# Optimization experiments

Hardware: AMD Instinct MI355X
Metric: run time of the kernel (lower is better)

Reference implementation:

```python
import jax
import jax.numpy as jnp
import numpy as np

N_NODES = 4096
N_EDGES = 65536
D_FEAT = 64


def setup_inputs() -> dict:
    key = jax.random.key(0)
    k1, k2, k3, k4 = jax.random.split(key, 4)
    x = jax.random.normal(k1, (N_NODES, D_FEAT), dtype=jnp.float32)
    edge_index = jax.random.randint(k2, (2, N_EDGES), 0, N_NODES, dtype=jnp.int32)
    batch = jnp.zeros((N_NODES,), dtype=jnp.int32)
    # GraphConv(in_channels, 1): lin_rel (with bias) on aggregated neighbors, lin_root on self
    w_rel = jax.random.normal(k3, (D_FEAT, 1), dtype=jnp.float32) * 0.1
    w_root = jax.random.normal(k4, (D_FEAT, 1), dtype=jnp.float32) * 0.1
    b = jnp.zeros((1,), dtype=jnp.float32)
    return {"x": x, "edge_index": edge_index, "batch": batch,
            "w_rel": w_rel, "w_root": w_root, "b": b}


def _merge_stars(x, src0, dst0, score):
    """Faithful sequential greedy star contraction (priority order by score desc)."""
    N = x.shape[0]
    order = jnp.argsort(-score)  # descending, ties like argsort

    def step(carry, node):
        xc, src, dst, remaining, center = carry
        active = remaining[node]
        # dests = set of targets of edges whose (current, rewritten) source == node,
        # minus already-chosen center nodes
        dest_edge = src == node                                  # [E]
        dest_node = jnp.zeros(N, bool).at[dst].max(dest_edge)    # node-level set
        dest_node = dest_node & ~center
        # torch does sum over list(dests)+[node]: node counted again (even on self-loop)
        combine = jnp.einsum('n,nd->d', dest_node.astype(xc.dtype), xc) + xc[node]
        D = dest_node.at[node].set(True)                         # dests U {node}
        x2 = xc.at[node].set(combine)
        src2 = jnp.where(D[src], node, src)                      # np.isin rewrite
        dst2 = jnp.where(D[dst], node, dst)
        rem2 = remaining & ~dest_node
        cen2 = center.at[node].set(True)
        carry2 = (jnp.where(active, x2, xc),
                  jnp.where(active, src2, src),
                  jnp.where(active, dst2, dst),
                  jnp.where(active, rem2, remaining),
                  jnp.where(active, cen2, center))
        return carry2, None

    init = (x, src0, dst0, jnp.ones(N, bool), jnp.zeros(N, bool))
    (x_final, _, _, remaining, _), _ = jax.lax.scan(step, init, order)
    return x_final, remaining


def reference(x, edge_index, batch, w_rel, w_root, b):
    N, d = x.shape
    src0, dst0 = edge_index[0], edge_index[1]
    # GraphConv score: W_rel * sum_{j->i} x_j + b + W_root * x_i ; dropout p=0; tanh
    agg = jax.ops.segment_sum(x[src0], dst0, num_segments=N)     # [N, d]
    score = jnp.tanh((agg @ w_rel + x @ w_root + b).reshape(-1)) # [N]

    x_final, remaining = _merge_stars(x, src0, dst0, score)

    # perm = sorted(nodes_remaining); outputs padded to static size N (sentinel -1)
    perm = jnp.nonzero(remaining, size=N, fill_value=N)[0]
    x_pooled = jnp.take(x_final, perm, axis=0, mode='fill', fill_value=0.0)
    kept = perm < N
    batch_pooled = jnp.where(kept, jnp.take(batch, jnp.minimum(perm, N - 1)), -1)
    # filter_adj on the ORIGINAL edge_index: keep edges with both endpoints kept,
    # relabel nodes to their rank among kept nodes; invalid edges -> -1
    relabel = jnp.cumsum(remaining.astype(jnp.int32)) - 1
    valid = remaining[src0] & remaining[dst0]
    new_src = jnp.where(valid, relabel[src0], -1)
    new_dst = jnp.where(valid, relabel[dst0], -1)
    new_edge_index = jnp.stack([new_src, new_dst])
    perm_out = jnp.where(kept, perm, -1)
    return x_pooled, new_edge_index, batch_pooled, perm_out
```

## Files before the change

### kernel.cpp

```cpp
#include <hip/hip_runtime.h>

#define NN 4096
#define NE 65536
#define ND 64

__global__ void k1_node_dots(const float* __restrict__ x, const float* __restrict__ wrel,
                             const float* __restrict__ wroot, double* __restrict__ srel,
                             double* __restrict__ sroot) {
    int gt = blockIdx.x * blockDim.x + threadIdx.x;
    int node = gt >> 6, lane = gt & 63;
    if (node >= NN) return;
    double xv = (double)x[node * ND + lane];
    double pr = xv * (double)wrel[lane];
    double po = xv * (double)wroot[lane];
    for (int off = 32; off > 0; off >>= 1) {
        pr += __shfl_down(pr, off);
        po += __shfl_down(po, off);
    }
    if (lane == 0) {
        srel[node] = pr;
        sroot[node] = po;
    }
}

__global__ void __launch_bounds__(1024) k34_contract(
        const double* __restrict__ srel, const double* __restrict__ sroot,
        const float* __restrict__ bptr, const int* __restrict__ ei,
        int* __restrict__ map_g, int* __restrict__ rem_g, int* __restrict__ relab_g,
        int* __restrict__ perm_a, int* __restrict__ nkeep_g) {
    __shared__ __align__(16) char buf[163840];
    unsigned short* incsr = (unsigned short*)buf;
    char* aux = buf + 131072;
    int* cursor = (int*)aux;
    double* srel_lds = (double*)aux;
    volatile unsigned long long* skey = (volatile unsigned long long*)aux;
    int* wt = (int*)(aux + 20544);
    int tid = threadIdx.x, lane = tid & 63, wv = tid >> 6;

    for (int n = tid; n < NN; n += 1024) cursor[n] = 0;
    __syncthreads();
    const int4* eid4 = (const int4*)(ei + NE);
    for (int i = tid; i < NE / 4; i += 1024) {
        int4 q = eid4[i];
        atomicAdd(&cursor[q.x], 1);
        atomicAdd(&cursor[q.y], 1);
        atomicAdd(&cursor[q.z], 1);
        atomicAdd(&cursor[q.w], 1);
    }
    __syncthreads();

    int t0 = cursor[4 * tid], t1 = cursor[4 * tid + 1];
    int t2 = cursor[4 * tid + 2], t3 = cursor[4 * tid + 3];
    int tot = t0 + t1 + t2 + t3;
    int inc = tot;
    for (int off = 1; off < 64; off <<= 1) {
        int v = __shfl_up(inc, off);
        if (lane >= off) inc += v;
    }
    if (lane == 63) wt[wv] = inc;
    __syncthreads();
    if (wv == 0 && lane < 16) {
        int v = wt[lane];
        for (int off = 1; off < 16; off <<= 1) {
            int u2 = __shfl_up(v, off);
            if (lane >= off) v += u2;
        }
        wt[lane] = v;
    }
    __syncthreads();
    int waveoff = (wv > 0) ? wt[wv - 1] : 0;
    int excl = waveoff + inc - tot;
    int rs4[4], re4[4];
    rs4[0] = excl; rs4[1] = excl + t0; rs4[2] = excl + t0 + t1; rs4[3] = excl + t0 + t1 + t2;
    cursor[4 * tid]     = rs4[0];
    cursor[4 * tid + 1] = rs4[1];
    cursor[4 * tid + 2] = rs4[2];
    cursor[4 * tid + 3] = rs4[3];
    __syncthreads();

    const int4* eis4 = (const int4*)ei;
    for (int i = tid; i < NE / 4; i += 1024) {
        int4 s = eis4[i];
        int4 d = eid4[i];
        incsr[atomicAdd(&cursor[d.x], 1)] = (unsigned short)s.x;
        incsr[atomicAdd(&cursor[d.y], 1)] = (unsigned short)s.y;
        incsr[atomicAdd(&cursor[d.z], 1)] = (unsigned short)s.z;
        incsr[atomicAdd(&cursor[d.w], 1)] = (unsigned short)s.w;
    }
    __syncthreads();
    for (int t = 0; t < 4; ++t) re4[t] = cursor[4 * tid + t];
    __syncthreads();

    {
        double2* sl2 = (double2*)aux;
        const double2* sg2 = (const double2*)srel;
        for (int i = tid; i < NN / 2; i += 1024) sl2[i] = sg2[i];
    }
    __syncthreads();

    double bv = (double)bptr[0];
    unsigned long long base4[4];
    for (int t = 0; t < 4; ++t) {
        int v = 4 * tid + t;
        double s = 0.0;
        for (int e = rs4[t]; e < re4[t]; ++e) s += srel_lds[(int)incsr[e]];
        double arg = s + sroot[v] + bv;
        float sc = tanhf((float)arg);
        unsigned m = __float_as_uint(sc);
        m = (m & 0x80000000u) ? ~m : (m | 0x80000000u);
        base4[t] = ((unsigned long long)(~m) << 14) | ((unsigned long long)v << 2);
    }
    __syncthreads();

    for (int t = 0; t < 4; ++t) skey[4 * tid + t] = base4[t];
    __syncthreads();

    unsigned long long pk4[4], minC4[4];
    unsigned resolved = 0, centerm = 0, selfm = 0;
    for (int t = 0; t < 4; ++t) {
        int v = 4 * tid + t;
        unsigned long long pkv = base4[t] >> 2;
        pk4[t] = pkv;
        minC4[t] = ~0ULL;
        int w = rs4[t];
        for (int e = rs4[t]; e < re4[t]; ++e) {
            int u = (int)incsr[e];
            if (u == v) { selfm |= 1u << t; continue; }
            unsigned long long ku = skey[u] >> 2;
            if (ku < pkv) incsr[w++] = (unsigned short)u;
        }
        re4[t] = w;
        if (w == rs4[t]) {
            map_g[v] = v;
            skey[v] = base4[t] | 1ULL;
            centerm |= 1u << t; resolved |= 1u << t;
        }
    }

    int guard = 0;
    while (resolved != 0xFu && guard < 1000000) {
        ++guard;
        bool prog = false;
        for (int t = 0; t < 4; ++t) {
            if (resolved & (1u << t)) continue;
            int v = 4 * tid + t;
            int lo = rs4[t], hi = re4[t];
            unsigned long long minU = ~0ULL, mC = minC4[t];
            int w = lo;
            for (int e = lo; e < hi; ++e) {
                int u = (int)incsr[e];
                unsigned long long sk = skey[u];
                int st = (int)(sk & 3ULL);
                unsigned long long ku = sk >> 2;
                if (st == 0) { incsr[w++] = (unsigned short)u; if (ku < minU) minU = ku; }
                else if (st == 1) { if (ku < mC) mC = ku; }
            }
            if (w != hi) prog = true;
            re4[t] = w; minC4[t] = mC;
            if (mC < minU) {
                map_g[v] = (int)((mC >> 2) & 0xFFFULL);
                skey[v] = (pk4[t] << 2) | 2ULL;
                resolved |= 1u << t; prog = true;
            } else if (w == lo) {
                map_g[v] = v;
                skey[v] = (pk4[t] << 2) | 1ULL;
                centerm |= 1u << t; resolved |= 1u << t; prog = true;
            }
        }
        if (!prog) __builtin_amdgcn_s_sleep(1);
    }
    __syncthreads();

    int remb[4], cnt4 = 0;
    for (int t = 0; t < 4; ++t) {
        remb[t] = ((centerm >> t) & 1) && !((selfm >> t) & 1);
        cnt4 += remb[t];
    }
    int inc2 = cnt4;
    for (int off = 1; off < 64; off <<= 1) {
        int v = __shfl_up(inc2, off);
        if (lane >= off) inc2 += v;
    }
    if (lane == 63) wt[wv] = inc2;
    __syncthreads();
    if (wv == 0 && lane < 16) {
        int v = wt[lane];
        for (int off = 1; off < 16; off <<= 1) {
            int u2 = __shfl_up(v, off);
            if (lane >= off) v += u2;
        }
        wt[lane] = v;
    }
    __syncthreads();
    int woff2 = (wv > 0) ? wt[wv - 1] : 0;
    int run = woff2 + inc2 - cnt4;
    for (int t = 0; t < 4; ++t) {
        int v = 4 * tid + t;
        relab_g[v] = run;
        if (remb[t]) { perm_a[run] = v; ++run; }
        rem_g[v] = remb[t];
    }
    if (tid == 1023) nkeep_g[0] = run;
}

__global__ void k56_outputs(const float* __restrict__ x, const int* __restrict__ map_g,
                            const int* __restrict__ rem_g, const int* __restrict__ relab_g,
                            const int* __restrict__ perm_a, const int* __restrict__ ei,
                            const int* __restrict__ batch, const int* __restrict__ nkeep_g,
                            float* __restrict__ out) {
    int idx = blockIdx.x * blockDim.x + threadIdx.x;
    if (idx < NN * ND) {
        int n = idx >> 6, d = idx & 63;
        int m = map_g[n];
        if (rem_g[m]) atomicAdd(&out[relab_g[m] * ND + d], x[idx]);
    } else if (idx < NN * ND + 2 * NE) {
        int e = idx - NN * ND;
        int row = e >> 16;
        int ee = e & (NE - 1);
        int s = ei[ee], t = ei[NE + ee];
        bool valid = (rem_g[s] != 0) && (rem_g[t] != 0);
        int endp = (row == 0) ? s : t;
        out[idx] = valid ? (float)relab_g[endp] : -1.0f;
    } else if (idx < NN * ND + 2 * NE + NN) {
        int r = idx - (NN * ND + 2 * NE);
        int nk = nkeep_g[0];
        out[idx] = (r < nk) ? (float)batch[perm_a[r]] : -1.0f;
    } else if (idx < NN * ND + 2 * NE + 2 * NN) {
        int r = idx - (NN * ND + 2 * NE + NN);
        int nk = nkeep_g[0];
        out[idx] = (r < nk) ? (float)perm_a[r] : -1.0f;
    }
}

extern "C" void kernel_launch(void* const* d_in, const int* in_sizes, int n_in,
                              void* d_out, int out_size, void* d_ws, size_t ws_size,
                              hipStream_t stream) {
    const float* x     = (const float*)d_in[0];
    const int*   ei    = (const int*)d_in[1];
    const int*   batch = (const int*)d_in[2];
    const float* wrel  = (const float*)d_in[3];
    const float* wroot = (const float*)d_in[4];
    const float* b     = (const float*)d_in[5];

    char* ws = (char*)d_ws;
    double* srel  = (double*)(ws + 0);
    double* sroot = (double*)(ws + 32768);
    int*    map_g = (int*)(ws + 65536);
    int*    rem_g = (int*)(ws + 81920);
    int*    relab = (int*)(ws + 98304);
    int*    perma = (int*)(ws + 114688);
    int*    nkeep = (int*)(ws + 131072);

    float* out = (float*)d_out;

    hipMemsetAsync(out, 0, NN * ND * sizeof(float), stream);
    k1_node_dots<<<NN * ND / 256, 256, 0, stream>>>(x, wrel, wroot, srel, sroot);
    k34_contract<<<1, 1024, 0, stream>>>(srel, sroot, b, ei, map_g, rem_g, relab,
                                         perma, nkeep);
    int total_out = NN * ND + 2 * NE + 2 * NN;
    k56_outputs<<<(total_out + 255) / 256, 256, 0, stream>>>(x, map_g, rem_g, relab,
                                                             perma, ei, batch, nkeep, out);
}
```

Measured before the change: 160.0 us.

## Sort higher-priority in-neighbors once and resolve greedy contraction via a status scan pointer

```diff
diff --git a/kernel.cpp b/kernel.cpp
--- a/kernel.cpp
+++ b/kernel.cpp
@@ -33,7 +33,8 @@
     char* aux = buf + 131072;
     int* cursor = (int*)aux;
     double* srel_lds = (double*)aux;
-    volatile unsigned long long* skey = (volatile unsigned long long*)aux;
+    unsigned* mono_s = (unsigned*)aux;
+    volatile unsigned char* stat_s = (volatile unsigned char*)(aux + 16384);
     int* wt = (int*)(aux + 20544);
     int tid = threadIdx.x, lane = tid & 63, wv = tid >> 6;
 
@@ -88,6 +89,7 @@
         incsr[atomicAdd(&cursor[d.w], 1)] = (unsigned short)s.w;
     }
     __syncthreads();
+    #pragma unroll
     for (int t = 0; t < 4; ++t) re4[t] = cursor[4 * tid + t];
     __syncthreads();
 
@@ -99,7 +101,8 @@
     __syncthreads();
 
     double bv = (double)bptr[0];
-    unsigned long long base4[4];
+    unsigned mono4[4];
+    #pragma unroll
     for (int t = 0; t < 4; ++t) {
         int v = 4 * tid + t;
         double s = 0.0;
@@ -108,32 +111,43 @@
         float sc = tanhf((float)arg);
         unsigned m = __float_as_uint(sc);
         m = (m & 0x80000000u) ? ~m : (m | 0x80000000u);
-        base4[t] = ((unsigned long long)(~m) << 14) | ((unsigned long long)v << 2);
-    }
-    __syncthreads();
-
-    for (int t = 0; t < 4; ++t) skey[4 * tid + t] = base4[t];
-    __syncthreads();
-
-    unsigned long long pk4[4], minC4[4];
+        mono4[t] = m;
+    }
+    __syncthreads();
+
+    #pragma unroll
+    for (int t = 0; t < 4; ++t) mono_s[4 * tid + t] = mono4[t];
+    ((int*)(aux + 16384))[tid] = 0;
+    __syncthreads();
+
     unsigned resolved = 0, centerm = 0, selfm = 0;
+    int pos4[4], fu4[4] = {0, 0, 0, 0};
+    #pragma unroll
     for (int t = 0; t < 4; ++t) {
         int v = 4 * tid + t;
-        unsigned long long pkv = base4[t] >> 2;
-        pk4[t] = pkv;
-        minC4[t] = ~0ULL;
-        int w = rs4[t];
-        for (int e = rs4[t]; e < re4[t]; ++e) {
+        unsigned mv = mono4[t];
+        int lo = rs4[t], w = lo;
+        for (int e = lo; e < re4[t]; ++e) {
             int u = (int)incsr[e];
             if (u == v) { selfm |= 1u << t; continue; }
-            unsigned long long ku = skey[u] >> 2;
-            if (ku < pkv) incsr[w++] = (unsigned short)u;
-        }
-        re4[t] = w;
-        if (w == rs4[t]) {
+            unsigned mu = mono_s[u];
+            if (!(mu > mv || (mu == mv && u < v))) continue;
+            int j = w;
+            while (j > lo) {
+                int q = (int)incsr[j - 1];
+                unsigned mq = mono_s[q];
+                if (mu > mq || (mu == mq && u < q)) { incsr[j] = (unsigned short)q; --j; }
+                else break;
+            }
+            incsr[j] = (unsigned short)u; ++w;
+        }
+        re4[t] = w; pos4[t] = lo;
+        if (w == lo) {
             map_g[v] = v;
-            skey[v] = base4[t] | 1ULL;
+            stat_s[v] = 1;
             centerm |= 1u << t; resolved |= 1u << t;
+        } else {
+            fu4[t] = (int)incsr[lo];
         }
     }
 
@@ -141,30 +155,34 @@
     while (resolved != 0xFu && guard < 1000000) {
         ++guard;
         bool prog = false;
+        #pragma unroll
         for (int t = 0; t < 4; ++t) {
             if (resolved & (1u << t)) continue;
             int v = 4 * tid + t;
-            int lo = rs4[t], hi = re4[t];
-            unsigned long long minU = ~0ULL, mC = minC4[t];
-            int w = lo;
-            for (int e = lo; e < hi; ++e) {
-                int u = (int)incsr[e];
-                unsigned long long sk = skey[u];
-                int st = (int)(sk & 3ULL);
-                unsigned long long ku = sk >> 2;
-                if (st == 0) { incsr[w++] = (unsigned short)u; if (ku < minU) minU = ku; }
-                else if (st == 1) { if (ku < mC) mC = ku; }
-            }
-            if (w != hi) prog = true;
-            re4[t] = w; minC4[t] = mC;
-            if (mC < minU) {
-                map_g[v] = (int)((mC >> 2) & 0xFFFULL);
-                skey[v] = (pk4[t] << 2) | 2ULL;
-                resolved |= 1u << t; prog = true;
-            } else if (w == lo) {
-                map_g[v] = v;
-                skey[v] = (pk4[t] << 2) | 1ULL;
-                centerm |= 1u << t; resolved |= 1u << t; prog = true;
+            int u = fu4[t];
+            int st = (int)stat_s[u];
+            if (st == 0) continue;
+            prog = true;
+            if (st == 1) {
+                map_g[v] = u; stat_s[v] = 2; resolved |= 1u << t; continue;
+            }
+            int p = pos4[t] + 1, hi = re4[t];
+            bool done = false;
+            while (p < hi) {
+                u = (int)incsr[p];
+                st = (int)stat_s[u];
+                if (st == 2) { ++p; continue; }
+                if (st == 1) {
+                    map_g[v] = u; stat_s[v] = 2; resolved |= 1u << t; done = true;
+                }
+                break;
+            }
+            if (!done) {
+                if (p >= hi) {
+                    map_g[v] = v; stat_s[v] = 1; centerm |= 1u << t; resolved |= 1u << t;
+                } else {
+                    pos4[t] = p; fu4[t] = u;
+                }
             }
         }
         if (!prog) __builtin_amdgcn_s_sleep(1);
@@ -172,6 +190,7 @@
     __syncthreads();
 
     int remb[4], cnt4 = 0;
+    #pragma unroll
     for (int t = 0; t < 4; ++t) {
         remb[t] = ((centerm >> t) & 1) && !((selfm >> t) & 1);
         cnt4 += remb[t];
@@ -194,6 +213,7 @@
     __syncthreads();
     int woff2 = (wv > 0) ? wt[wv - 1] : 0;
     int run = woff2 + inc2 - cnt4;
+    #pragma unroll
     for (int t = 0; t < 4; ++t) {
         int v = 4 * tid + t;
         relab_g[v] = run;
```

Result: slower. 410.1 us (+156.3%).
